# Optimization experiments

Measured on AMD Instinct MI355X. Metric: run time of the kernel, lower is better.

Reference implementation:

```python
import jax, jax.numpy as jnp
import numpy as np

D_IN = 4096
D_OUT = 4096
RANK = 16
ALPHA = 32
SCALE = ALPHA / RANK


def setup_inputs() -> dict:
    key = jax.random.key(0)
    k_x, k_w, k_b, k_a = jax.random.split(key, 4)
    x = jax.random.normal(k_x, (4, 2048, D_IN), dtype=jnp.float32)
    weight = jax.random.normal(k_w, (D_OUT, D_IN), dtype=jnp.float32) * (1.0 / np.sqrt(D_IN))
    bias = jax.random.normal(k_b, (D_OUT,), dtype=jnp.float32)
    lora_A = jax.random.normal(k_a, (RANK, D_IN), dtype=jnp.float32) * 0.01
    lora_B = jnp.zeros((D_OUT, RANK), dtype=jnp.float32)
    return {"x": x, "weight": weight, "bias": bias, "lora_A": lora_A, "lora_B": lora_B}


def reference(x, weight, bias, lora_A, lora_B):
    # base linear: y = x @ W^T + b   -> [B, S, D_OUT]
    orig_out = jnp.einsum("bsd,od->bso", x, weight) + bias
    # low-rank path: (x @ A^T) @ B^T * (alpha/rank)
    lora_out = jnp.einsum("bsr,or->bso", jnp.einsum("bsd,rd->bsr", x, lora_A), lora_B)
    return orig_out + lora_out * SCALE
```

## Files before the change

### kernel.cpp

```cpp
#include <hip/hip_runtime.h>
#include <stdint.h>

#define DIN   4096
#define DOUT  4096
#define RANK  16
#define MTOT  8192
#define LSCALE 2.0f

typedef unsigned short u16;
typedef __bf16 bf16x8 __attribute__((ext_vector_type(8)));
typedef float  f32x4  __attribute__((ext_vector_type(4)));
typedef u16    u16x8  __attribute__((ext_vector_type(8)));

__device__ __forceinline__ u16 f2bf(float f) {
    uint32_t u = __builtin_bit_cast(uint32_t, f);
    u = (u + 0x7FFFu + ((u >> 16) & 1u)) >> 16;
    return (u16)u;
}

__device__ __forceinline__ u16x8 pack8(f32x4 a, f32x4 b) {
    u16x8 o;
    o[0] = f2bf(a[0]); o[1] = f2bf(a[1]); o[2] = f2bf(a[2]); o[3] = f2bf(a[3]);
    o[4] = f2bf(b[0]); o[5] = f2bf(b[1]); o[6] = f2bf(b[2]); o[7] = f2bf(b[3]);
    return o;
}

#define GLDS16(g, l) __builtin_amdgcn_global_load_lds( \
    (const __attribute__((address_space(1))) void*)(g), \
    (__attribute__((address_space(3))) void*)(l), 16, 0, 0)

__global__ __launch_bounds__(256) void k_convert_x(const float* __restrict__ x,
                                                   u16* __restrict__ xb) {
    long i = ((long)blockIdx.x * 256 + threadIdx.x) * 8;
    f32x4 a = *(const f32x4*)(x + i);
    f32x4 b = *(const f32x4*)(x + i + 4);
    *(u16x8*)(xb + i) = pack8(a, b);
}

__global__ __launch_bounds__(256) void k_build_weff(const float* __restrict__ W,
                                                    const float* __restrict__ A,
                                                    const float* __restrict__ B,
                                                    u16* __restrict__ wb) {
    long t = (long)blockIdx.x * 256 + threadIdx.x;
    long i = t * 8;
    int o = (int)(i >> 12);
    int d = (int)(i & (DIN - 1));
    float sB[RANK];
#pragma unroll
    for (int r = 0; r < RANK; ++r) sB[r] = B[o * RANK + r] * LSCALE;
    f32x4 w0 = *(const f32x4*)(W + i);
    f32x4 w1 = *(const f32x4*)(W + i + 4);
#pragma unroll
    for (int r = 0; r < RANK; ++r) {
        f32x4 a0 = *(const f32x4*)(A + (long)r * DIN + d);
        f32x4 a1 = *(const f32x4*)(A + (long)r * DIN + d + 4);
        w0 += a0 * sB[r];
        w1 += a1 * sB[r];
    }
    *(u16x8*)(wb + i) = pack8(w0, w1);
}

#define BM 256
#define BN 256
#define BK 64
#define NT (DIN / BK)

#define MFMA16(d, a, b) d = __builtin_amdgcn_mfma_f32_16x16x32_bf16(a, b, d, 0, 0, 0)
#define RAWBAR() __builtin_amdgcn_s_barrier()
#define VMCNT4() asm volatile("s_waitcnt vmcnt(4)" ::: "memory")

__global__ __launch_bounds__(512, 2) void k_gemm_ws(const u16* __restrict__ xb,
                                                    const u16* __restrict__ wb,
                                                    const float* __restrict__ bias,
                                                    float* __restrict__ out) {
    constexpr int K = DIN, N = DOUT;
    __shared__ alignas(16) u16 lds[65536];

    const int nchunk = gridDim.x >> 3;
    const int bid = blockIdx.x;
    const int wg  = (bid & 7) * nchunk + (bid >> 3);
    const int bm  = (wg & 31) * BM;
    const int bn  = (wg >> 5) * BN;

    const int tid  = threadIdx.x;
    const int lane = tid & 63;
    const int wid  = tid >> 6;
    const int wr   = wid >> 2;
    const int wc   = wid & 3;
    const int lrow = lane & 15;
    const int kgrp = lane >> 4;

    const int srow = tid >> 3;
    const int sgl  = (tid & 7) ^ (srow & 7);
    const u16* const aSrcB = xb + (long)(bm + srow) * K + sgl * 8;
    const u16* const bSrcB = wb + (long)(bn + srow) * K + sgl * 8;

#define STAGE_A(c, buf, kt) GLDS16(aSrcB + (long)(64*(c))*K + (kt)*BK, \
                                   lds + (buf)*16384 + (c)*4096 + tid*8)
#define STAGE_B(c, buf, kt) GLDS16(bSrcB + (long)(64*(c))*K + (kt)*BK, \
                                   lds + 32768 + (buf)*16384 + (c)*4096 + tid*8)

    const int go0 = (kgrp ^ (lrow & 7)) * 8;
    const int go1 = go0 ^ 32;
    const int arL = (wr*64 + lrow) * 64;
    const int arH = arL + 128*64;
    const int brL = (wc*32 + lrow) * 64;
    const int brH = brL + 128*64;

    f32x4 acc[8][4];
#pragma unroll
    for (int m = 0; m < 8; ++m)
#pragma unroll
        for (int n = 0; n < 4; ++n) acc[m][n] = (f32x4){0.f, 0.f, 0.f, 0.f};

    STAGE_A(0, 0, 0); STAGE_A(1, 0, 0);
    STAGE_B(0, 0, 0); STAGE_B(1, 0, 0);
    STAGE_B(2, 0, 0); STAGE_B(3, 0, 0);
    STAGE_A(2, 0, 0); STAGE_A(3, 0, 0);
    asm volatile("s_waitcnt vmcnt(0)" ::: "memory");
    __syncthreads();

    for (int t = 0; t < NT; ++t) {
        const int cur = t & 1, nxt = cur ^ 1;
        const int tn = (t + 1) & (NT - 1);
        const u16* const pA = lds + cur*16384;
        const u16* const pB = lds + 32768 + cur*16384;

        bf16x8 afL[4][2], afH[4][2], bfA[2][2], bfB[2][2];

#pragma unroll
        for (int m = 0; m < 4; ++m) {
            afL[m][0] = *(const bf16x8*)(pA + arL + m*1024 + go0);
            afL[m][1] = *(const bf16x8*)(pA + arL + m*1024 + go1);
        }
#pragma unroll
        for (int n = 0; n < 2; ++n) {
            bfA[n][0] = *(const bf16x8*)(pB + brL + n*1024 + go0);
            bfA[n][1] = *(const bf16x8*)(pB + brL + n*1024 + go1);
        }
        STAGE_A(0, nxt, tn); STAGE_A(1, nxt, tn);
        RAWBAR();
        __builtin_amdgcn_s_setprio(1);
#pragma unroll
        for (int m = 0; m < 4; ++m)
#pragma unroll
            for (int n = 0; n < 2; ++n) {
                MFMA16(acc[m][n], afL[m][0], bfA[n][0]);
                MFMA16(acc[m][n], afL[m][1], bfA[n][1]);
            }
        __builtin_amdgcn_s_setprio(0);
        VMCNT4();
        RAWBAR();

#pragma unroll
        for (int n = 0; n < 2; ++n) {
            bfB[n][0] = *(const bf16x8*)(pB + brH + n*1024 + go0);
            bfB[n][1] = *(const bf16x8*)(pB + brH + n*1024 + go1);
        }
        STAGE_B(0, nxt, tn); STAGE_B(1, nxt, tn);
        RAWBAR();
        __builtin_amdgcn_s_setprio(1);
#pragma unroll
        for (int m = 0; m < 4; ++m)
#pragma unroll
            for (int n = 0; n < 2; ++n) {
                MFMA16(acc[m][n+2], afL[m][0], bfB[n][0]);
                MFMA16(acc[m][n+2], afL[m][1], bfB[n][1]);
            }
        __builtin_amdgcn_s_setprio(0);
        VMCNT4();
        RAWBAR();

#pragma unroll
        for (int m = 0; m < 4; ++m) {
            afH[m][0] = *(const bf16x8*)(pA + arH + m*1024 + go0);
            afH[m][1] = *(const bf16x8*)(pA + arH + m*1024 + go1);
        }
        STAGE_B(2, nxt, tn); STAGE_B(3, nxt, tn);
        RAWBAR();
        __builtin_amdgcn_s_setprio(1);
#pragma unroll
        for (int m = 0; m < 4; ++m)
#pragma unroll
            for (int n = 0; n < 2; ++n) {
                MFMA16(acc[m+4][n+2], afH[m][0], bfB[n][0]);
                MFMA16(acc[m+4][n+2], afH[m][1], bfB[n][1]);
            }
        __builtin_amdgcn_s_setprio(0);
        RAWBAR();

        STAGE_A(2, nxt, tn); STAGE_A(3, nxt, tn);
        RAWBAR();
        __builtin_amdgcn_s_setprio(1);
#pragma unroll
        for (int m = 0; m < 4; ++m)
#pragma unroll
            for (int n = 0; n < 2; ++n) {
                MFMA16(acc[m+4][n], afH[m][0], bfA[n][0]);
                MFMA16(acc[m+4][n], afH[m][1], bfA[n][1]);
            }
        __builtin_amdgcn_s_setprio(0);
        VMCNT4();
        RAWBAR();
    }
    asm volatile("s_waitcnt vmcnt(0)" ::: "memory");

    const int orow = bm + wr*64 + kgrp*4;
    const int ocol = bn + wc*32 + lrow;
#pragma unroll
    for (int n = 0; n < 4; ++n) {
        const int col = ocol + (n & 1)*16 + (n >> 1)*128;
        const float bj = bias[col];
#pragma unroll
        for (int m = 0; m < 8; ++m) {
            const int row = orow + (m & 3)*16 + (m >> 2)*128;
#pragma unroll
            for (int r = 0; r < 4; ++r)
                out[(long)(row + r) * N + col] = acc[m][n][r] + bj;
        }
    }
}

__global__ __launch_bounds__(64) void k_lora_T(const float* __restrict__ x,
                                               const float* __restrict__ A,
                                               float* __restrict__ T) {
    const int m = blockIdx.x;
    const int lane = threadIdx.x;
    const float* xr = x + (long)m * DIN;
    float acc[RANK];
#pragma unroll
    for (int r = 0; r < RANK; ++r) acc[r] = 0.f;
    for (int k = lane * 4; k < DIN; k += 64 * 4) {
        f32x4 xv = *(const f32x4*)(xr + k);
#pragma unroll
        for (int r = 0; r < RANK; ++r) {
            f32x4 av = *(const f32x4*)(A + (long)r * DIN + k);
            acc[r] += xv[0] * av[0] + xv[1] * av[1] + xv[2] * av[2] + xv[3] * av[3];
        }
    }
#pragma unroll
    for (int r = 0; r < RANK; ++r)
        for (int off = 32; off > 0; off >>= 1) acc[r] += __shfl_down(acc[r], off);
    if (lane == 0) {
#pragma unroll
        for (int r = 0; r < RANK; ++r) T[(long)m * RANK + r] = acc[r] * LSCALE;
    }
}

__global__ __launch_bounds__(256) void k_gemm_nows(const float* __restrict__ x,
                                                   const float* __restrict__ W,
                                                   const float* __restrict__ bias,
                                                   const float* __restrict__ T,
                                                   const float* __restrict__ lB,
                                                   float* __restrict__ out) {
    constexpr int FBM = 128, FBN = 128, FBK = 32, K = DIN, N = DOUT;
    __shared__ __align__(16) u16 As[FBM * FBK];
    __shared__ __align__(16) u16 Bs[FBN * FBK];

    const int tid = threadIdx.x;
    const int bm = blockIdx.y * FBM;
    const int bn = blockIdx.x * FBN;
    const int lane = tid & 63;
    const int wid  = tid >> 6;
    const int wr = wid >> 1, wc = wid & 1;
    const int lrow = lane & 15;
    const int kgrp = lane >> 4;

    const int c0 = tid, c1 = tid + 256;
    const float* aS0 = x + (long)(bm + (c0 >> 2)) * K + (c0 & 3) * 8;
    const float* aS1 = x + (long)(bm + (c1 >> 2)) * K + (c1 & 3) * 8;
    const float* bS0 = W + (long)(bn + (c0 >> 2)) * K + (c0 & 3) * 8;
    const float* bS1 = W + (long)(bn + (c1 >> 2)) * K + (c1 & 3) * 8;
    u16* aD0 = As + c0 * 8;  u16* aD1 = As + c1 * 8;
    u16* bD0 = Bs + c0 * 8;  u16* bD1 = Bs + c1 * 8;

    const u16* aR = As + (wr * 64 + lrow) * FBK + kgrp * 8;
    const u16* bR = Bs + (wc * 64 + lrow) * FBK + kgrp * 8;

    f32x4 acc[4][4];
#pragma unroll
    for (int i = 0; i < 4; ++i)
#pragma unroll
        for (int j = 0; j < 4; ++j) acc[i][j] = (f32x4){0.f, 0.f, 0.f, 0.f};

    for (int k0 = 0; k0 < K; k0 += FBK) {
        f32x4 a00 = *(const f32x4*)aS0, a01 = *(const f32x4*)(aS0 + 4);
        f32x4 a10 = *(const f32x4*)aS1, a11 = *(const f32x4*)(aS1 + 4);
        f32x4 b00 = *(const f32x4*)bS0, b01 = *(const f32x4*)(bS0 + 4);
        f32x4 b10 = *(const f32x4*)bS1, b11 = *(const f32x4*)(bS1 + 4);
        aS0 += FBK; aS1 += FBK; bS0 += FBK; bS1 += FBK;
        if (k0) __syncthreads();
        *(u16x8*)aD0 = pack8(a00, a01);
        *(u16x8*)aD1 = pack8(a10, a11);
        *(u16x8*)bD0 = pack8(b00, b01);
        *(u16x8*)bD1 = pack8(b10, b11);
        __syncthreads();

        bf16x8 af[4], bf[4];
#pragma unroll
        for (int i = 0; i < 4; ++i) af[i] = *(const bf16x8*)(aR + i * 16 * FBK);
#pragma unroll
        for (int j = 0; j < 4; ++j) bf[j] = *(const bf16x8*)(bR + j * 16 * FBK);
#pragma unroll
        for (int i = 0; i < 4; ++i)
#pragma unroll
            for (int j = 0; j < 4; ++j)
                acc[i][j] = __builtin_amdgcn_mfma_f32_16x16x32_bf16(af[i], bf[j], acc[i][j], 0, 0, 0);
    }

#pragma unroll
    for (int j = 0; j < 4; ++j) {
        const int col = bn + wc * 64 + j * 16 + lrow;
        const float bj = bias[col];
        float bl[RANK];
#pragma unroll
        for (int q = 0; q < RANK; ++q) bl[q] = lB[(long)col * RANK + q];
#pragma unroll
        for (int i = 0; i < 4; ++i) {
            const int row0 = bm + wr * 64 + i * 16 + kgrp * 4;
#pragma unroll
            for (int r = 0; r < 4; ++r) {
                const int row = row0 + r;
                const float* Trow = T + (long)row * RANK;
                float s = bj;
#pragma unroll
                for (int q = 0; q < RANK; ++q) s += Trow[q] * bl[q];
                out[(long)row * N + col] = acc[i][j][r] + s;
            }
        }
    }
}

extern "C" void kernel_launch(void* const* d_in, const int* in_sizes, int n_in,
                              void* d_out, int out_size, void* d_ws, size_t ws_size,
                              hipStream_t stream) {
    const float* x    = (const float*)d_in[0];
    const float* W    = (const float*)d_in[1];
    const float* bias = (const float*)d_in[2];
    const float* lA   = (const float*)d_in[3];
    const float* lB   = (const float*)d_in[4];
    float* out = (float*)d_out;

    const size_t xb_bytes = (size_t)MTOT * DIN * sizeof(u16);
    const size_t wb_bytes = (size_t)DOUT * DIN * sizeof(u16);

    if (ws_size >= xb_bytes + wb_bytes) {
        u16* xb = (u16*)d_ws;
        u16* wb = (u16*)((char*)d_ws + xb_bytes);
        k_convert_x <<<(int)((long)MTOT * DIN / 8 / 256), 256, 0, stream>>>(x, xb);
        k_build_weff<<<(int)((long)DOUT * DIN / 8 / 256), 256, 0, stream>>>(W, lA, lB, wb);
        k_gemm_ws   <<<(MTOT / BM) * (DOUT / BN), 512, 0, stream>>>(xb, wb, bias, out);
    } else {
        float* T = (float*)d_ws;
        k_lora_T   <<<MTOT, 64, 0, stream>>>(x, lA, T);
        k_gemm_nows<<<dim3(DOUT / 128, MTOT / 128), 256, 0, stream>>>(x, W, bias, T, lB, out);
    }
}
```

Measured before the change: 331.1 us.

## Restructure GEMM main loop into unrolled two-tile software pipeline with prefetched fragments

Unrolls the K loop by two with fixed LDS buffer pointers. LDS fragment reads for the next quadrant, including the next tile's A-low and B-low fragments, are issued before the current quadrant's MFMAs. Each phase now has a single vmcnt(2) wait plus one barrier, replacing the old two barriers per phase with vmcnt(4). The aim is to hide LDS read latency behind MFMA work and cut synchronization overhead. In exchange it uses more fragment registers and relies on the tighter wait counts and buffer reuse ordering being correct.

Result: slower. 376.9 us (+13.8%).

```diff
diff --git a/kernel.cpp b/kernel.cpp
--- a/kernel.cpp
+++ b/kernel.cpp
@@ -66,8 +66,33 @@
 #define NT (DIN / BK)
 
 #define MFMA16(d, a, b) d = __builtin_amdgcn_mfma_f32_16x16x32_bf16(a, b, d, 0, 0, 0)
-#define RAWBAR() __builtin_amdgcn_s_barrier()
-#define VMCNT4() asm volatile("s_waitcnt vmcnt(4)" ::: "memory")
+#define GATE2() asm volatile("s_waitcnt vmcnt(2)" ::: "memory")
+#define ABAR()  asm volatile("s_barrier" ::: "memory")
+#define PRIO1() __builtin_amdgcn_s_setprio(1)
+#define PRIO0() __builtin_amdgcn_s_setprio(0)
+
+#define QUAD(mo, no, AF, BF) \
+    _Pragma("unroll") \
+    for (int m = 0; m < 4; ++m) { \
+        _Pragma("unroll") \
+        for (int n = 0; n < 2; ++n) { \
+            MFMA16(acc[(mo)+m][(no)+n], AF[m][0], BF[n][0]); \
+            MFMA16(acc[(mo)+m][(no)+n], AF[m][1], BF[n][1]); \
+        } \
+    }
+
+#define READ_A4(DST, P, RB) \
+    _Pragma("unroll") \
+    for (int m = 0; m < 4; ++m) { \
+        DST[m][0] = *(const bf16x8*)((P) + (RB) + m*1024 + go0); \
+        DST[m][1] = *(const bf16x8*)((P) + (RB) + m*1024 + go1); \
+    }
+#define READ_B2(DST, P, RB) \
+    _Pragma("unroll") \
+    for (int n = 0; n < 2; ++n) { \
+        DST[n][0] = *(const bf16x8*)((P) + (RB) + n*1024 + go0); \
+        DST[n][1] = *(const bf16x8*)((P) + (RB) + n*1024 + go1); \
+    }
 
 __global__ __launch_bounds__(512, 2) void k_gemm_ws(const u16* __restrict__ xb,
                                                     const u16* __restrict__ wb,
@@ -107,101 +132,71 @@
     const int brL = (wc*32 + lrow) * 64;
     const int brH = brL + 128*64;
 
+    const u16* const pA0 = lds;
+    const u16* const pA1 = lds + 16384;
+    const u16* const pB0 = lds + 32768;
+    const u16* const pB1 = lds + 49152;
+
     f32x4 acc[8][4];
 #pragma unroll
     for (int m = 0; m < 8; ++m)
 #pragma unroll
         for (int n = 0; n < 4; ++n) acc[m][n] = (f32x4){0.f, 0.f, 0.f, 0.f};
+
+    bf16x8 afL[4][2], afH[4][2], bfB[2][2], bfAe[2][2], bfAo[2][2];
 
     STAGE_A(0, 0, 0); STAGE_A(1, 0, 0);
     STAGE_B(0, 0, 0); STAGE_B(1, 0, 0);
     STAGE_B(2, 0, 0); STAGE_B(3, 0, 0);
     STAGE_A(2, 0, 0); STAGE_A(3, 0, 0);
     asm volatile("s_waitcnt vmcnt(0)" ::: "memory");
-    __syncthreads();
-
-    for (int t = 0; t < NT; ++t) {
-        const int cur = t & 1, nxt = cur ^ 1;
-        const int tn = (t + 1) & (NT - 1);
-        const u16* const pA = lds + cur*16384;
-        const u16* const pB = lds + 32768 + cur*16384;
-
-        bf16x8 afL[4][2], afH[4][2], bfA[2][2], bfB[2][2];
-
-#pragma unroll
-        for (int m = 0; m < 4; ++m) {
-            afL[m][0] = *(const bf16x8*)(pA + arL + m*1024 + go0);
-            afL[m][1] = *(const bf16x8*)(pA + arL + m*1024 + go1);
-        }
-#pragma unroll
-        for (int n = 0; n < 2; ++n) {
-            bfA[n][0] = *(const bf16x8*)(pB + brL + n*1024 + go0);
-            bfA[n][1] = *(const bf16x8*)(pB + brL + n*1024 + go1);
-        }
-        STAGE_A(0, nxt, tn); STAGE_A(1, nxt, tn);
-        RAWBAR();
-        __builtin_amdgcn_s_setprio(1);
-#pragma unroll
-        for (int m = 0; m < 4; ++m)
-#pragma unroll
-            for (int n = 0; n < 2; ++n) {
-                MFMA16(acc[m][n], afL[m][0], bfA[n][0]);
-                MFMA16(acc[m][n], afL[m][1], bfA[n][1]);
-            }
-        __builtin_amdgcn_s_setprio(0);
-        VMCNT4();
-        RAWBAR();
-
-#pragma unroll
-        for (int n = 0; n < 2; ++n) {
-            bfB[n][0] = *(const bf16x8*)(pB + brH + n*1024 + go0);
-            bfB[n][1] = *(const bf16x8*)(pB + brH + n*1024 + go1);
-        }
-        STAGE_B(0, nxt, tn); STAGE_B(1, nxt, tn);
-        RAWBAR();
-        __builtin_amdgcn_s_setprio(1);
-#pragma unroll
-        for (int m = 0; m < 4; ++m)
-#pragma unroll
-            for (int n = 0; n < 2; ++n) {
-                MFMA16(acc[m][n+2], afL[m][0], bfB[n][0]);
-                MFMA16(acc[m][n+2], afL[m][1], bfB[n][1]);
-            }
-        __builtin_amdgcn_s_setprio(0);
-        VMCNT4();
-        RAWBAR();
-
-#pragma unroll
-        for (int m = 0; m < 4; ++m) {
-            afH[m][0] = *(const bf16x8*)(pA + arH + m*1024 + go0);
-            afH[m][1] = *(const bf16x8*)(pA + arH + m*1024 + go1);
-        }
-        STAGE_B(2, nxt, tn); STAGE_B(3, nxt, tn);
-        RAWBAR();
-        __builtin_amdgcn_s_setprio(1);
-#pragma unroll
-        for (int m = 0; m < 4; ++m)
-#pragma unroll
-            for (int n = 0; n < 2; ++n) {
-                MFMA16(acc[m+4][n+2], afH[m][0], bfB[n][0]);
-                MFMA16(acc[m+4][n+2], afH[m][1], bfB[n][1]);
-            }
-        __builtin_amdgcn_s_setprio(0);
-        RAWBAR();
-
-        STAGE_A(2, nxt, tn); STAGE_A(3, nxt, tn);
-        RAWBAR();
-        __builtin_amdgcn_s_setprio(1);
-#pragma unroll
-        for (int m = 0; m < 4; ++m)
-#pragma unroll
-            for (int n = 0; n < 2; ++n) {
-                MFMA16(acc[m+4][n], afH[m][0], bfA[n][0]);
-                MFMA16(acc[m+4][n], afH[m][1], bfA[n][1]);
-            }
-        __builtin_amdgcn_s_setprio(0);
-        VMCNT4();
-        RAWBAR();
+    ABAR();
+    READ_A4(afL, pA0, arL);
+    READ_B2(bfAe, pB0, brL);
+
+    for (int it = 0; it < NT/2; ++it) {
+        const int tn0 = 2*it + 1;
+        const int tn1 = (2*it + 2) & (NT - 1);
+
+        GATE2(); ABAR();
+        READ_B2(bfB, pB0, brH);
+        STAGE_A(0, 1, tn0); STAGE_A(1, 1, tn0);
+        PRIO1(); QUAD(0, 0, afL, bfAe); PRIO0();
+
+        GATE2(); ABAR();
+        READ_A4(afH, pA0, arH);
+        STAGE_B(0, 1, tn0); STAGE_B(1, 1, tn0);
+        PRIO1(); QUAD(0, 2, afL, bfB); PRIO0();
+
+        GATE2(); ABAR();
+        READ_A4(afL, pA1, arL);
+        STAGE_B(2, 1, tn0); STAGE_B(3, 1, tn0);
+        PRIO1(); QUAD(4, 2, afH, bfB); PRIO0();
+
+        GATE2(); ABAR();
+        READ_B2(bfAo, pB1, brL);
+        STAGE_A(2, 1, tn0); STAGE_A(3, 1, tn0);
+        PRIO1(); QUAD(4, 0, afH, bfAe); PRIO0();
+
+        GATE2(); ABAR();
+        READ_B2(bfB, pB1, brH);
+        STAGE_A(0, 0, tn1); STAGE_A(1, 0, tn1);
+        PRIO1(); QUAD(0, 0, afL, bfAo); PRIO0();
+
+        GATE2(); ABAR();
+        READ_A4(afH, pA1, arH);
+        STAGE_B(0, 0, tn1); STAGE_B(1, 0, tn1);
+        PRIO1(); QUAD(0, 2, afL, bfB); PRIO0();
+
+        GATE2(); ABAR();
+        READ_A4(afL, pA0, arL);
+        STAGE_B(2, 0, tn1); STAGE_B(3, 0, tn1);
+        PRIO1(); QUAD(4, 2, afH, bfB); PRIO0();
+
+        GATE2(); ABAR();
+        READ_B2(bfAe, pB0, brL);
+        STAGE_A(2, 0, tn1); STAGE_A(3, 0, tn1);
+        PRIO1(); QUAD(4, 0, afH, bfAo); PRIO0();
     }
     asm volatile("s_waitcnt vmcnt(0)" ::: "memory");
 
```
